# Optimization experiments

Measured on AMD Instinct MI355X. Metric: run time of the kernel, lower is better.

The kernel has to match this reference:

```python
import jax, jax.numpy as jnp
import numpy as np

PPSZ = 256  # default in CLIMB; npix = 3*PPSZ = 768
EPS = 1e-15


def _lsq_matrix():
    # Constant 3x9 pseudo-inverse for planar least-squares fit on a 3x3 patch
    xx, yy = np.meshgrid(np.linspace(0.0, 1.0, 3), np.linspace(0.0, 1.0, 3))
    A = np.vstack([xx.ravel(), yy.ravel(), np.ones(9)]).T  # (9,3)
    M = np.linalg.inv(A.T @ A) @ A.T  # (3,9)
    return jnp.asarray(M, dtype=jnp.float32)

_M = _lsq_matrix()


def _area(flat):
    # flat: (N, 9) flattened 3x3 patches; vectorized version of per-patch `area`
    params = flat @ _M.T  # (N,3) -> a, b, c of plane fit
    a, b, c = params[:, 0], params[:, 1], params[:, 2]
    a = jnp.where(a == 0, EPS, a)
    b = jnp.where(b == 0, EPS, b)
    c = jnp.where(c == 0, EPS, c)
    x1 = (-b - c) / a
    x2 = -c / a
    lo = jnp.minimum(x1, x2)
    hi = jnp.maximum(x1, x2)
    x1 = jnp.maximum(lo, 0.0)
    x2 = jnp.minimum(hi, 1.0)
    d = x1 + (-c / b) * x2 - 0.5 * (a / b) * x2 ** 2 - (-c / b) * x1 + 0.5 * (a / b) * x1 ** 2
    d = jnp.where(d >= 0.5, d, 1.0 - d)
    d = jnp.where(jnp.mean(flat, axis=1) >= 0, d, 1.0 - d)
    d = jnp.where(jnp.all(flat > 0, axis=1), 1.0, d)
    d = jnp.where(jnp.all(flat <= 0, axis=1), 0.0, d)
    d = jnp.where(jnp.any(flat == 0, axis=1), (d > 0).astype(d.dtype), d)
    return jnp.clip(d, 0.0, 1.0)


def _climb(wf, ppsz=PPSZ):
    # Reproduce wf.split(ppsz) then split(ppsz, axis=2): dummy[c, r] = wf[3r:3r+3, 3c:3c+3]
    patches = wf.reshape(ppsz, 3, ppsz, 3).transpose(2, 0, 1, 3)  # (ppsz, ppsz, 3, 3)
    flat = patches.reshape(-1, 9)
    return _area(flat).reshape(ppsz, ppsz)


def setup_inputs() -> dict:
    key = jax.random.key(0)
    k1, k2 = jax.random.split(key)
    nterms, npix = 128, 3 * PPSZ
    basis = jax.random.normal(k1, (nterms, npix, npix), dtype=jnp.float32)
    coeffs = jax.random.normal(k2, (nterms,), dtype=jnp.float32)
    ideal_wavel = jnp.asarray(1e-6, dtype=jnp.float32)
    return {"basis": basis, "coeffs": coeffs, "ideal_wavel": ideal_wavel}


def reference(basis, coeffs, ideal_wavel):
    # get_opd: np.dot(basis.T, coeffs) -> result[i,j] = sum_n basis[n,j,i]*coeffs[n]
    latent = jnp.einsum("nij,n->ji", basis, coeffs)  # (768, 768)
    binary_phase = jnp.pi * _climb(latent)  # (256, 256)
    opd = binary_phase * ideal_wavel / (2.0 * jnp.pi)
    return opd
```

## Files before the change

kernel.cpp:

```cpp
#include <hip/hip_runtime.h>

#define NPIX   768
#define PP     256
#define NTERMS 128
#define EPSF   1e-15f

typedef float f32x4 __attribute__((ext_vector_type(4)));

#define NV4   (NPIX * NPIX / 4)

__global__ __launch_bounds__(64) void latent_kernel(
    const float* __restrict__ basis,
    const float* __restrict__ coeffs,
    float* __restrict__ W)
{
    __shared__ float sc[NTERMS];
    sc[threadIdx.x]      = coeffs[threadIdx.x];
    sc[threadIdx.x + 64] = coeffs[threadIdx.x + 64];
    __syncthreads();

    const int t0 = blockIdx.x * 192 + threadIdx.x;
    const f32x4* __restrict__ b4 = (const f32x4*)basis;

    f32x4 a0 = {0.f, 0.f, 0.f, 0.f};
    f32x4 a1 = {0.f, 0.f, 0.f, 0.f};
    f32x4 a2 = {0.f, 0.f, 0.f, 0.f};

    #pragma unroll 1
    for (int n = 0; n < NTERMS; n += 2) {
        const f32x4* __restrict__ pa = b4 + (long)n * NV4 + t0;
        const f32x4* __restrict__ pb = pa + NV4;
        f32x4 v0 = __builtin_nontemporal_load(pa);
        f32x4 v1 = __builtin_nontemporal_load(pa + 64);
        f32x4 v2 = __builtin_nontemporal_load(pa + 128);
        f32x4 v3 = __builtin_nontemporal_load(pb);
        f32x4 v4 = __builtin_nontemporal_load(pb + 64);
        f32x4 v5 = __builtin_nontemporal_load(pb + 128);

        const float ca = sc[n];
        const float cb = sc[n + 1];
        a0.x = fmaf(v0.x, ca, a0.x); a0.y = fmaf(v0.y, ca, a0.y);
        a0.z = fmaf(v0.z, ca, a0.z); a0.w = fmaf(v0.w, ca, a0.w);
        a1.x = fmaf(v1.x, ca, a1.x); a1.y = fmaf(v1.y, ca, a1.y);
        a1.z = fmaf(v1.z, ca, a1.z); a1.w = fmaf(v1.w, ca, a1.w);
        a2.x = fmaf(v2.x, ca, a2.x); a2.y = fmaf(v2.y, ca, a2.y);
        a2.z = fmaf(v2.z, ca, a2.z); a2.w = fmaf(v2.w, ca, a2.w);
        a0.x = fmaf(v3.x, cb, a0.x); a0.y = fmaf(v3.y, cb, a0.y);
        a0.z = fmaf(v3.z, cb, a0.z); a0.w = fmaf(v3.w, cb, a0.w);
        a1.x = fmaf(v4.x, cb, a1.x); a1.y = fmaf(v4.y, cb, a1.y);
        a1.z = fmaf(v4.z, cb, a1.z); a1.w = fmaf(v4.w, cb, a1.w);
        a2.x = fmaf(v5.x, cb, a2.x); a2.y = fmaf(v5.y, cb, a2.y);
        a2.z = fmaf(v5.z, cb, a2.z); a2.w = fmaf(v5.w, cb, a2.w);
    }

    f32x4* __restrict__ W4 = (f32x4*)W;
    W4[t0]       = a0;
    W4[t0 + 64]  = a1;
    W4[t0 + 128] = a2;
}

__device__ __forceinline__ float climb_area(const float f[9])
{
    float sum = 0.f;
    #pragma unroll
    for (int m = 0; m < 9; ++m) sum += f[m];
    float mean = sum * (1.f / 9.f);

    float a = (f[2] + f[5] + f[8] - f[0] - f[3] - f[6]) * (1.f / 3.f);
    float b = (f[6] + f[7] + f[8] - f[0] - f[1] - f[2]) * (1.f / 3.f);
    float c = mean - 0.5f * (a + b);

    if (a == 0.f) a = EPSF;
    if (b == 0.f) b = EPSF;
    if (c == 0.f) c = EPSF;

    float x1 = (-b - c) / a;
    float x2 = -c / a;
    float lo = fminf(x1, x2);
    float hi = fmaxf(x1, x2);
    x1 = fmaxf(lo, 0.f);
    x2 = fminf(hi, 1.f);

    float cb = -c / b;
    float ab = 0.5f * (a / b);
    float d = x1 + cb * x2 - ab * x2 * x2 - cb * x1 + ab * x1 * x1;

    d = (d >= 0.5f) ? d : 1.f - d;
    d = (mean >= 0.f) ? d : 1.f - d;

    bool allpos = true, allnp = true, anyz = false;
    #pragma unroll
    for (int m = 0; m < 9; ++m) {
        allpos = allpos && (f[m] > 0.f);
        allnp  = allnp  && (f[m] <= 0.f);
        anyz   = anyz   || (f[m] == 0.f);
    }
    if (allpos) d = 1.f;
    if (allnp)  d = 0.f;
    if (anyz)   d = (d > 0.f) ? 1.f : 0.f;

    return fminf(fmaxf(d, 0.f), 1.f);
}

__global__ __launch_bounds__(256) void climb_kernel(
    const float* __restrict__ W,
    const float* __restrict__ wavel,
    float* __restrict__ out)
{
    const int t = blockIdx.x * 256 + threadIdx.x;
    const int r = t >> 8;
    const int p = t & 255;

    const float* __restrict__ base = W + (3 * r) * NPIX + 3 * p;
    float f[9];
    #pragma unroll
    for (int s = 0; s < 3; ++s)
        #pragma unroll
        for (int q = 0; q < 3; ++q)
            f[q * 3 + s] = base[s * NPIX + q];

    out[t] = climb_area(f) * 0.5f * wavel[0];
}

__global__ __launch_bounds__(256) void fused_kernel(
    const float* __restrict__ basis,
    const float* __restrict__ coeffs,
    const float* __restrict__ wavel,
    float* __restrict__ out)
{
    __shared__ float sc[NTERMS];
    if (threadIdx.x < NTERMS) sc[threadIdx.x] = coeffs[threadIdx.x];
    __syncthreads();

    const int t = blockIdx.x * 256 + threadIdx.x;
    const int r = t >> 8;
    const int p = t & 255;

    const float* __restrict__ base = basis + (3 * r) * NPIX + 3 * p;
    float f[9];
    #pragma unroll
    for (int m = 0; m < 9; ++m) f[m] = 0.f;

    for (int n = 0; n < NTERMS; ++n) {
        const float* __restrict__ bn = base + (long)n * NPIX * NPIX;
        float cn = sc[n];
        #pragma unroll
        for (int s = 0; s < 3; ++s)
            #pragma unroll
            for (int q = 0; q < 3; ++q)
                f[q * 3 + s] = fmaf(bn[s * NPIX + q], cn, f[q * 3 + s]);
    }

    out[t] = climb_area(f) * 0.5f * wavel[0];
}

extern "C" void kernel_launch(void* const* d_in, const int* in_sizes, int n_in,
                              void* d_out, int out_size, void* d_ws, size_t ws_size,
                              hipStream_t stream)
{
    const float* basis  = (const float*)d_in[0];
    const float* coeffs = (const float*)d_in[1];
    const float* wavel  = (const float*)d_in[2];
    float* out = (float*)d_out;

    const size_t w_bytes = (size_t)NPIX * NPIX * sizeof(float);
    if (ws_size >= w_bytes) {
        float* W = (float*)d_ws;
        latent_kernel<<<NV4 / 192, 64, 0, stream>>>(basis, coeffs, W);
        climb_kernel<<<(PP * PP) / 256, 256, 0, stream>>>(W, wavel, out);
    } else {
        fused_kernel<<<(PP * PP) / 256, 256, 0, stream>>>(basis, coeffs, wavel, out);
    }
}
```

Before: 374.4 us.

## Restructure latent reduction: one vec4 per thread, 8-term unrolled loads, 256-thread blocks

Reworks the basis-coefficient reduction so each thread owns one float4 pixel group and loads eight terms per iteration, with two interleaved accumulators. Blocks grow from 64 to 256 threads, which triples the total thread count and raises memory-level parallelism on this bandwidth-bound stream. Plain loads replace the nontemporal loads. The summation order changes slightly.

```diff
diff --git a/kernel.cpp b/kernel.cpp
--- a/kernel.cpp
+++ b/kernel.cpp
@@ -9,54 +9,61 @@
 
 #define NV4   (NPIX * NPIX / 4)
 
-__global__ __launch_bounds__(64) void latent_kernel(
+__global__ __launch_bounds__(256) void latent_kernel(
     const float* __restrict__ basis,
     const float* __restrict__ coeffs,
     float* __restrict__ W)
 {
     __shared__ float sc[NTERMS];
-    sc[threadIdx.x]      = coeffs[threadIdx.x];
-    sc[threadIdx.x + 64] = coeffs[threadIdx.x + 64];
+    if (threadIdx.x < NTERMS) sc[threadIdx.x] = coeffs[threadIdx.x];
     __syncthreads();
 
-    const int t0 = blockIdx.x * 192 + threadIdx.x;
-    const f32x4* __restrict__ b4 = (const f32x4*)basis;
+    const int t = blockIdx.x * 256 + threadIdx.x;
+    const f32x4* __restrict__ b4 = (const f32x4*)basis + t;
 
-    f32x4 a0 = {0.f, 0.f, 0.f, 0.f};
-    f32x4 a1 = {0.f, 0.f, 0.f, 0.f};
-    f32x4 a2 = {0.f, 0.f, 0.f, 0.f};
+    f32x4 acc0 = {0.f, 0.f, 0.f, 0.f};
+    f32x4 acc1 = {0.f, 0.f, 0.f, 0.f};
 
     #pragma unroll 1
-    for (int n = 0; n < NTERMS; n += 2) {
-        const f32x4* __restrict__ pa = b4 + (long)n * NV4 + t0;
-        const f32x4* __restrict__ pb = pa + NV4;
-        f32x4 v0 = __builtin_nontemporal_load(pa);
-        f32x4 v1 = __builtin_nontemporal_load(pa + 64);
-        f32x4 v2 = __builtin_nontemporal_load(pa + 128);
-        f32x4 v3 = __builtin_nontemporal_load(pb);
-        f32x4 v4 = __builtin_nontemporal_load(pb + 64);
-        f32x4 v5 = __builtin_nontemporal_load(pb + 128);
+    for (int n = 0; n < NTERMS; n += 8) {
+        f32x4 v0 = b4[(long)(n + 0) * NV4];
+        f32x4 v1 = b4[(long)(n + 1) * NV4];
+        f32x4 v2 = b4[(long)(n + 2) * NV4];
+        f32x4 v3 = b4[(long)(n + 3) * NV4];
+        f32x4 v4 = b4[(long)(n + 4) * NV4];
+        f32x4 v5 = b4[(long)(n + 5) * NV4];
+        f32x4 v6 = b4[(long)(n + 6) * NV4];
+        f32x4 v7 = b4[(long)(n + 7) * NV4];
 
-        const float ca = sc[n];
-        const float cb = sc[n + 1];
-        a0.x = fmaf(v0.x, ca, a0.x); a0.y = fmaf(v0.y, ca, a0.y);
-        a0.z = fmaf(v0.z, ca, a0.z); a0.w = fmaf(v0.w, ca, a0.w);
-        a1.x = fmaf(v1.x, ca, a1.x); a1.y = fmaf(v1.y, ca, a1.y);
-        a1.z = fmaf(v1.z, ca, a1.z); a1.w = fmaf(v1.w, ca, a1.w);
-        a2.x = fmaf(v2.x, ca, a2.x); a2.y = fmaf(v2.y, ca, a2.y);
-        a2.z = fmaf(v2.z, ca, a2.z); a2.w = fmaf(v2.w, ca, a2.w);
-        a0.x = fmaf(v3.x, cb, a0.x); a0.y = fmaf(v3.y, cb, a0.y);
-        a0.z = fmaf(v3.z, cb, a0.z); a0.w = fmaf(v3.w, cb, a0.w);
-        a1.x = fmaf(v4.x, cb, a1.x); a1.y = fmaf(v4.y, cb, a1.y);
-        a1.z = fmaf(v4.z, cb, a1.z); a1.w = fmaf(v4.w, cb, a1.w);
-        a2.x = fmaf(v5.x, cb, a2.x); a2.y = fmaf(v5.y, cb, a2.y);
-        a2.z = fmaf(v5.z, cb, a2.z); a2.w = fmaf(v5.w, cb, a2.w);
+        const float c0 = sc[n + 0];
+        const float c1 = sc[n + 1];
+        const float c2 = sc[n + 2];
+        const float c3 = sc[n + 3];
+        const float c4 = sc[n + 4];
+        const float c5 = sc[n + 5];
+        const float c6 = sc[n + 6];
+        const float c7 = sc[n + 7];
+
+        acc0.x = fmaf(v0.x, c0, acc0.x); acc0.y = fmaf(v0.y, c0, acc0.y);
+        acc0.z = fmaf(v0.z, c0, acc0.z); acc0.w = fmaf(v0.w, c0, acc0.w);
+        acc1.x = fmaf(v1.x, c1, acc1.x); acc1.y = fmaf(v1.y, c1, acc1.y);
+        acc1.z = fmaf(v1.z, c1, acc1.z); acc1.w = fmaf(v1.w, c1, acc1.w);
+        acc0.x = fmaf(v2.x, c2, acc0.x); acc0.y = fmaf(v2.y, c2, acc0.y);
+        acc0.z = fmaf(v2.z, c2, acc0.z); acc0.w = fmaf(v2.w, c2, acc0.w);
+        acc1.x = fmaf(v3.x, c3, acc1.x); acc1.y = fmaf(v3.y, c3, acc1.y);
+        acc1.z = fmaf(v3.z, c3, acc1.z); acc1.w = fmaf(v3.w, c3, acc1.w);
+        acc0.x = fmaf(v4.x, c4, acc0.x); acc0.y = fmaf(v4.y, c4, acc0.y);
+        acc0.z = fmaf(v4.z, c4, acc0.z); acc0.w = fmaf(v4.w, c4, acc0.w);
+        acc1.x = fmaf(v5.x, c5, acc1.x); acc1.y = fmaf(v5.y, c5, acc1.y);
+        acc1.z = fmaf(v5.z, c5, acc1.z); acc1.w = fmaf(v5.w, c5, acc1.w);
+        acc0.x = fmaf(v6.x, c6, acc0.x); acc0.y = fmaf(v6.y, c6, acc0.y);
+        acc0.z = fmaf(v6.z, c6, acc0.z); acc0.w = fmaf(v6.w, c6, acc0.w);
+        acc1.x = fmaf(v7.x, c7, acc1.x); acc1.y = fmaf(v7.y, c7, acc1.y);
+        acc1.z = fmaf(v7.z, c7, acc1.z); acc1.w = fmaf(v7.w, c7, acc1.w);
     }
 
     f32x4* __restrict__ W4 = (f32x4*)W;
-    W4[t0]       = a0;
-    W4[t0 + 64]  = a1;
-    W4[t0 + 128] = a2;
+    W4[t] = acc0 + acc1;
 }
 
 __device__ __forceinline__ float climb_area(const float f[9])
@@ -166,7 +173,7 @@
     const size_t w_bytes = (size_t)NPIX * NPIX * sizeof(float);
     if (ws_size >= w_bytes) {
         float* W = (float*)d_ws;
-        latent_kernel<<<NV4 / 192, 64, 0, stream>>>(basis, coeffs, W);
+        latent_kernel<<<NV4 / 256, 256, 0, stream>>>(basis, coeffs, W);
         climb_kernel<<<(PP * PP) / 256, 256, 0, stream>>>(W, wavel, out);
     } else {
         fused_kernel<<<(PP * PP) / 256, 256, 0, stream>>>(basis, coeffs, wavel, out);
```

After: 400.0 us. +6.8%, slower.

## Fuse latent reduction and climb into one kernel with LDS triple-buffered async loads

Applied to the files above, without the earlier changes.

Replaces the two-kernel path (latent reduction into a workspace, then the patch area kernel) with a single fused kernel. Each block handles one 3-row strip of the image and streams the matching 2304-float slice of every basis plane into LDS through global_load_lds, using a three-slot ring with s_waitcnt and barriers. Each thread then accumulates its 3x3 patch from LDS. This removes the workspace write and re-read and the second launch. The cost is only 256 blocks, which limits how many loads are in flight for a kernel bound by memory bandwidth, plus two barriers per term.

```diff
diff --git a/kernel.cpp b/kernel.cpp
--- a/kernel.cpp
+++ b/kernel.cpp
@@ -4,60 +4,12 @@
 #define PP     256
 #define NTERMS 128
 #define EPSF   1e-15f
+#define PLANEF (NPIX * NPIX)
+#define ROWF   (3 * NPIX)
 
 typedef float f32x4 __attribute__((ext_vector_type(4)));
-
-#define NV4   (NPIX * NPIX / 4)
-
-__global__ __launch_bounds__(64) void latent_kernel(
-    const float* __restrict__ basis,
-    const float* __restrict__ coeffs,
-    float* __restrict__ W)
-{
-    __shared__ float sc[NTERMS];
-    sc[threadIdx.x]      = coeffs[threadIdx.x];
-    sc[threadIdx.x + 64] = coeffs[threadIdx.x + 64];
-    __syncthreads();
-
-    const int t0 = blockIdx.x * 192 + threadIdx.x;
-    const f32x4* __restrict__ b4 = (const f32x4*)basis;
-
-    f32x4 a0 = {0.f, 0.f, 0.f, 0.f};
-    f32x4 a1 = {0.f, 0.f, 0.f, 0.f};
-    f32x4 a2 = {0.f, 0.f, 0.f, 0.f};
-
-    #pragma unroll 1
-    for (int n = 0; n < NTERMS; n += 2) {
-        const f32x4* __restrict__ pa = b4 + (long)n * NV4 + t0;
-        const f32x4* __restrict__ pb = pa + NV4;
-        f32x4 v0 = __builtin_nontemporal_load(pa);
-        f32x4 v1 = __builtin_nontemporal_load(pa + 64);
-        f32x4 v2 = __builtin_nontemporal_load(pa + 128);
-        f32x4 v3 = __builtin_nontemporal_load(pb);
-        f32x4 v4 = __builtin_nontemporal_load(pb + 64);
-        f32x4 v5 = __builtin_nontemporal_load(pb + 128);
-
-        const float ca = sc[n];
-        const float cb = sc[n + 1];
-        a0.x = fmaf(v0.x, ca, a0.x); a0.y = fmaf(v0.y, ca, a0.y);
-        a0.z = fmaf(v0.z, ca, a0.z); a0.w = fmaf(v0.w, ca, a0.w);
-        a1.x = fmaf(v1.x, ca, a1.x); a1.y = fmaf(v1.y, ca, a1.y);
-        a1.z = fmaf(v1.z, ca, a1.z); a1.w = fmaf(v1.w, ca, a1.w);
-        a2.x = fmaf(v2.x, ca, a2.x); a2.y = fmaf(v2.y, ca, a2.y);
-        a2.z = fmaf(v2.z, ca, a2.z); a2.w = fmaf(v2.w, ca, a2.w);
-        a0.x = fmaf(v3.x, cb, a0.x); a0.y = fmaf(v3.y, cb, a0.y);
-        a0.z = fmaf(v3.z, cb, a0.z); a0.w = fmaf(v3.w, cb, a0.w);
-        a1.x = fmaf(v4.x, cb, a1.x); a1.y = fmaf(v4.y, cb, a1.y);
-        a1.z = fmaf(v4.z, cb, a1.z); a1.w = fmaf(v4.w, cb, a1.w);
-        a2.x = fmaf(v5.x, cb, a2.x); a2.y = fmaf(v5.y, cb, a2.y);
-        a2.z = fmaf(v5.z, cb, a2.z); a2.w = fmaf(v5.w, cb, a2.w);
-    }
-
-    f32x4* __restrict__ W4 = (f32x4*)W;
-    W4[t0]       = a0;
-    W4[t0 + 64]  = a1;
-    W4[t0 + 128] = a2;
-}
+typedef __attribute__((address_space(1))) const void* gas_p;
+typedef __attribute__((address_space(3))) void*       las_p;
 
 __device__ __forceinline__ float climb_area(const float f[9])
 {
@@ -102,26 +54,6 @@
     return fminf(fmaxf(d, 0.f), 1.f);
 }
 
-__global__ __launch_bounds__(256) void climb_kernel(
-    const float* __restrict__ W,
-    const float* __restrict__ wavel,
-    float* __restrict__ out)
-{
-    const int t = blockIdx.x * 256 + threadIdx.x;
-    const int r = t >> 8;
-    const int p = t & 255;
-
-    const float* __restrict__ base = W + (3 * r) * NPIX + 3 * p;
-    float f[9];
-    #pragma unroll
-    for (int s = 0; s < 3; ++s)
-        #pragma unroll
-        for (int q = 0; q < 3; ++q)
-            f[q * 3 + s] = base[s * NPIX + q];
-
-    out[t] = climb_area(f) * 0.5f * wavel[0];
-}
-
 __global__ __launch_bounds__(256) void fused_kernel(
     const float* __restrict__ basis,
     const float* __restrict__ coeffs,
@@ -129,29 +61,78 @@
     float* __restrict__ out)
 {
     __shared__ float sc[NTERMS];
-    if (threadIdx.x < NTERMS) sc[threadIdx.x] = coeffs[threadIdx.x];
+    __shared__ float lds[3][ROWF];
+
+    const int tid  = threadIdx.x;
+    const int lane = tid & 63;
+    const int wv   = tid >> 6;
+    const int r    = blockIdx.x;
+
+    if (tid < NTERMS) sc[tid] = coeffs[tid];
     __syncthreads();
 
-    const int t = blockIdx.x * 256 + threadIdx.x;
-    const int r = t >> 8;
-    const int p = t & 255;
+    const float* __restrict__ gbase = basis + (size_t)r * ROWF;
 
-    const float* __restrict__ base = basis + (3 * r) * NPIX + 3 * p;
+    #define STAGE(sl, pl) do {                                                  \
+        const float* gs_ = gbase + (size_t)(pl) * PLANEF;                       \
+        __builtin_amdgcn_global_load_lds(                                       \
+            (gas_p)(gs_ + (wv << 8) + (lane << 2)),                             \
+            (las_p)(&lds[(sl)][(wv) << 8]), 16, 0, 0);                          \
+        __builtin_amdgcn_global_load_lds(                                       \
+            (gas_p)(gs_ + 1024 + (wv << 8) + (lane << 2)),                      \
+            (las_p)(&lds[(sl)][1024 + ((wv) << 8)]), 16, 0, 0);                 \
+        __builtin_amdgcn_global_load_lds(                                       \
+            (gas_p)(gs_ + 2048 + (wv << 6) + lane),                             \
+            (las_p)(&lds[(sl)][2048 + ((wv) << 6)]), 4, 0, 0);                  \
+    } while (0)
+
+    #define COMPUTE(n_, sl_) do {                                               \
+        const float cn_ = sc[(n_)];                                             \
+        const float* __restrict__ L_ = lds[(sl_)];                              \
+        _Pragma("unroll")                                                       \
+        for (int s_ = 0; s_ < 3; ++s_)                                          \
+            _Pragma("unroll")                                                   \
+            for (int q_ = 0; q_ < 3; ++q_)                                      \
+                f[q_ * 3 + s_] = fmaf(L_[s_ * NPIX + x0 + q_], cn_,             \
+                                      f[q_ * 3 + s_]);                          \
+    } while (0)
+
     float f[9];
     #pragma unroll
     for (int m = 0; m < 9; ++m) f[m] = 0.f;
+    const int x0 = 3 * tid;
 
-    for (int n = 0; n < NTERMS; ++n) {
-        const float* __restrict__ bn = base + (long)n * NPIX * NPIX;
-        float cn = sc[n];
-        #pragma unroll
-        for (int s = 0; s < 3; ++s)
-            #pragma unroll
-            for (int q = 0; q < 3; ++q)
-                f[q * 3 + s] = fmaf(bn[s * NPIX + q], cn, f[q * 3 + s]);
+    STAGE(0, 0);
+    STAGE(1, 1);
+
+    int cur = 0, nxt = 2;
+    #pragma unroll 1
+    for (int n = 0; n < NTERMS - 2; ++n) {
+        STAGE(nxt, n + 2);
+        asm volatile("s_waitcnt vmcnt(6)" ::: "memory");
+        __builtin_amdgcn_s_barrier();
+        COMPUTE(n, cur);
+        asm volatile("" ::: "memory");
+        __builtin_amdgcn_s_barrier();
+        cur = (cur == 2) ? 0 : cur + 1;
+        nxt = (nxt == 2) ? 0 : nxt + 1;
     }
 
-    out[t] = climb_area(f) * 0.5f * wavel[0];
+    asm volatile("s_waitcnt vmcnt(3)" ::: "memory");
+    __builtin_amdgcn_s_barrier();
+    COMPUTE(NTERMS - 2, cur);
+    asm volatile("" ::: "memory");
+    __builtin_amdgcn_s_barrier();
+    cur = (cur == 2) ? 0 : cur + 1;
+
+    asm volatile("s_waitcnt vmcnt(0)" ::: "memory");
+    __builtin_amdgcn_s_barrier();
+    COMPUTE(NTERMS - 1, cur);
+
+    out[r * PP + tid] = climb_area(f) * 0.5f * wavel[0];
+
+    #undef STAGE
+    #undef COMPUTE
 }
 
 extern "C" void kernel_launch(void* const* d_in, const int* in_sizes, int n_in,
@@ -162,13 +143,7 @@
     const float* coeffs = (const float*)d_in[1];
     const float* wavel  = (const float*)d_in[2];
     float* out = (float*)d_out;
+    (void)d_ws; (void)ws_size;
 
-    const size_t w_bytes = (size_t)NPIX * NPIX * sizeof(float);
-    if (ws_size >= w_bytes) {
-        float* W = (float*)d_ws;
-        latent_kernel<<<NV4 / 192, 64, 0, stream>>>(basis, coeffs, W);
-        climb_kernel<<<(PP * PP) / 256, 256, 0, stream>>>(W, wavel, out);
-    } else {
-        fused_kernel<<<(PP * PP) / 256, 256, 0, stream>>>(basis, coeffs, wavel, out);
-    }
+    fused_kernel<<<PP, 256, 0, stream>>>(basis, coeffs, wavel, out);
 }
```

Measured after the change: 417.1 us. 11.4% more time.
